# Kernel optimization log

Measured on AMD Instinct MI355X. Metric: run time of the kernel, lower is better.

## Reference

```python
import jax, jax.numpy as jnp
import numpy as np

WINDOW_SIZE = 11
SIGMA = 1.5
C1 = 0.01 ** 2
C2 = 0.03 ** 2
MSE_WEIGHT = 1.0
SSIM_WEIGHT = 0.01


def _gaussian_window(channels):
    # 1D gaussian, normalized, then outer product -> [C,1,K,K] depthwise kernel
    coords = np.arange(WINDOW_SIZE) - WINDOW_SIZE // 2
    g = np.exp(-(coords ** 2) / (2.0 * SIGMA ** 2))
    g = g / g.sum()
    w2d = np.outer(g, g).astype(np.float32)  # [K,K]
    w = np.tile(w2d[None, None], (channels, 1, 1, 1))  # [C,1,K,K]
    return jnp.asarray(w)


def _depthwise_conv(x, w):
    # x: [B,C,H,W], w: [C,1,K,K]; SAME padding, groups=C (matches torch conv2d pad=K//2, groups=C)
    pad = WINDOW_SIZE // 2
    return jax.lax.conv_general_dilated(
        x, w,
        window_strides=(1, 1),
        padding=[(pad, pad), (pad, pad)],
        dimension_numbers=('NCHW', 'OIHW', 'NCHW'),
        feature_group_count=x.shape[1],
    )


def setup_inputs() -> dict:
    key = jax.random.key(0)
    k1, k2 = jax.random.split(key)
    shape = (32, 3, 512, 512)
    predicted = jax.random.uniform(k1, shape, dtype=jnp.float32)
    target = jax.random.uniform(k2, shape, dtype=jnp.float32)
    return {"predicted": predicted, "target": target}


def reference(predicted, target):
    # MSE part
    mse_l = jnp.mean((predicted - target) ** 2)

    # SSIM part (standard pytorch-ssim: gaussian window, size_average=True)
    C = predicted.shape[1]
    w = _gaussian_window(C)

    mu1 = _depthwise_conv(predicted, w)
    mu2 = _depthwise_conv(target, w)
    mu1_sq = mu1 * mu1
    mu2_sq = mu2 * mu2
    mu1_mu2 = mu1 * mu2

    sigma1_sq = _depthwise_conv(predicted * predicted, w) - mu1_sq
    sigma2_sq = _depthwise_conv(target * target, w) - mu2_sq
    sigma12 = _depthwise_conv(predicted * target, w) - mu1_mu2

    ssim_map = ((2.0 * mu1_mu2 + C1) * (2.0 * sigma12 + C2)) / (
        (mu1_sq + mu2_sq + C1) * (sigma1_sq + sigma2_sq + C2)
    )
    ssim_val = jnp.mean(ssim_map)

    return MSE_WEIGHT * mse_l + SSIM_WEIGHT * (1.0 - ssim_val)
```

## Files before the change

### kernel.cpp

```cpp
#include <hip/hip_runtime.h>
#include <hip/hip_fp16.h>


#define WSZ   512
#define TW    64
#define TH    16
#define HALO  5
#define IN_H  (TH + 2*HALO)
#define NPOS  32
#define GX    (WSZ / TW)
#define GY    (WSZ / TH)
#define NSLOT 64
#define SSIM_C1 0.0001f
#define SSIM_C2 0.0009f

#define W0 0.00102838f
#define W1 0.00759876f
#define W2 0.03600080f
#define W3 0.10936080f
#define W4 0.21300560f
#define W5 0.26601170f
__device__ __constant__ const float GW[11] = {W0,W1,W2,W3,W4,W5,W4,W3,W2,W1,W0};

static __device__ __forceinline__ float pkh2(float a, float b) {
    return __builtin_bit_cast(float, __builtin_amdgcn_cvt_pkrtz(a, b));
}

__launch_bounds__(256, 8)
__global__ void fused_mse_ssim(const float* __restrict__ P,
                               const float* __restrict__ T,
                               float* __restrict__ ws) {
    __shared__ float4 sAB[IN_H][NPOS];
    __shared__ float  sC [IN_H][NPOS];
    __shared__ float  red[2][4];

    const int tid = threadIdx.x;
    const int gx0 = blockIdx.x * TW;
    const int gy0 = blockIdx.y * TH;
    const size_t plane = (size_t)blockIdx.z * (WSZ * (size_t)WSZ);
    const float* Pp = P + plane;
    const float* Tp = T + plane;

    float gw[11];
    #pragma unroll
    for (int k = 0; k < 11; ++k) gw[k] = GW[k];

    float mse = 0.f;

    for (int it = tid; it < IN_H * 16; it += 256) {
        const int r = it >> 4;
        const int q = it & 15;
        const int gy = gy0 - HALO + r;
        const int c0 = gx0 + q * 4 - 8;
        const bool rv = ((unsigned)gy < (unsigned)WSZ);
        const float* prow = Pp + (size_t)gy * WSZ;
        const float* trow = Tp + (size_t)gy * WSZ;

        float p[20], t[20];
        #pragma unroll
        for (int b = 0; b < 5; ++b) {
            const int c = c0 + 4 * b;
            float4 pv = make_float4(0.f, 0.f, 0.f, 0.f);
            float4 tv = make_float4(0.f, 0.f, 0.f, 0.f);
            if (rv && ((unsigned)c < (unsigned)WSZ)) {
                pv = *(const float4*)(prow + c);
                tv = *(const float4*)(trow + c);
            }
            p[4*b+0] = pv.x; p[4*b+1] = pv.y; p[4*b+2] = pv.z; p[4*b+3] = pv.w;
            t[4*b+0] = tv.x; t[4*b+1] = tv.y; t[4*b+2] = tv.z; t[4*b+3] = tv.w;
        }

        if ((unsigned)(r - HALO) < (unsigned)TH) {
            #pragma unroll
            for (int i = 0; i < 4; ++i) {
                const float d = p[8 + i] - t[8 + i];
                mse = fmaf(d, d, mse);
            }
        }

        float aP[4]  = {0.f,0.f,0.f,0.f};
        float aT[4]  = {0.f,0.f,0.f,0.f};
        float aPP[4] = {0.f,0.f,0.f,0.f};
        float aTT[4] = {0.f,0.f,0.f,0.f};
        float aPT[4] = {0.f,0.f,0.f,0.f};
        #pragma unroll
        for (int jj = 0; jj < 14; ++jj) {
            const float pv = p[jj + 3];
            const float tv = t[jj + 3];
            const float pp = pv * pv, tt2 = tv * tv, pt = pv * tv;
            #pragma unroll
            for (int o = 0; o < 4; ++o) {
                const int k = jj - o;
                if (k >= 0 && k < 11) {
                    const float w = gw[k];
                    aP[o]  = fmaf(w, pv,  aP[o]);
                    aT[o]  = fmaf(w, tv,  aT[o]);
                    aPP[o] = fmaf(w, pp,  aPP[o]);
                    aTT[o] = fmaf(w, tt2, aTT[o]);
                    aPT[o] = fmaf(w, pt,  aPT[o]);
                }
            }
        }

        sAB[r][2*q]   = make_float4(pkh2(aP[0], aP[1]), pkh2(aT[0], aT[1]),
                                    pkh2(aPP[0],aPP[1]), pkh2(aTT[0],aTT[1]));
        sAB[r][2*q+1] = make_float4(pkh2(aP[2], aP[3]), pkh2(aT[2], aT[3]),
                                    pkh2(aPP[2],aPP[3]), pkh2(aTT[2],aTT[3]));
        sC [r][2*q]   = pkh2(aPT[0], aPT[1]);
        sC [r][2*q+1] = pkh2(aPT[2], aPT[3]);
    }
    __syncthreads();

    __half2 gwh[11];
    #pragma unroll
    for (int k = 0; k < 11; ++k) gwh[k] = __float2half2_rn(gw[k]);

    const int q2 = tid & 31;
    const int y0 = (tid >> 5) * 2;

    __half2 acc[2][5];
    #pragma unroll
    for (int a = 0; a < 2; ++a)
        #pragma unroll
        for (int f = 0; f < 5; ++f)
            acc[a][f] = __float2half2_rn(0.f);

    #pragma unroll
    for (int j = 0; j < 12; ++j) {
        const float4 ab = sAB[y0 + j][q2];
        const float  cc = sC [y0 + j][q2];
        __half2 h[5];
        h[0] = __builtin_bit_cast(__half2, ab.x);
        h[1] = __builtin_bit_cast(__half2, ab.y);
        h[2] = __builtin_bit_cast(__half2, ab.z);
        h[3] = __builtin_bit_cast(__half2, ab.w);
        h[4] = __builtin_bit_cast(__half2, cc);
        if (j < 11) {
            #pragma unroll
            for (int f = 0; f < 5; ++f) acc[0][f] = __hfma2(gwh[j], h[f], acc[0][f]);
        }
        if (j >= 1) {
            #pragma unroll
            for (int f = 0; f < 5; ++f) acc[1][f] = __hfma2(gwh[j-1], h[f], acc[1][f]);
        }
    }

    float ssim = 0.f;
    #pragma unroll
    for (int a = 0; a < 2; ++a) {
        const float2 m1  = __half22float2(acc[a][0]);
        const float2 m2  = __half22float2(acc[a][1]);
        const float2 spp = __half22float2(acc[a][2]);
        const float2 stt = __half22float2(acc[a][3]);
        const float2 spt = __half22float2(acc[a][4]);
        #pragma unroll
        for (int e = 0; e < 2; ++e) {
            const float mu1 = e ? m1.y  : m1.x;
            const float mu2 = e ? m2.y  : m2.x;
            const float vpp = e ? spp.y : spp.x;
            const float vtt = e ? stt.y : stt.x;
            const float vpt = e ? spt.y : spt.x;
            const float mu1sq = mu1 * mu1;
            const float mu2sq = mu2 * mu2;
            const float mu12  = mu1 * mu2;
            const float s1  = vpp - mu1sq;
            const float s2  = vtt - mu2sq;
            const float s12 = vpt - mu12;
            const float num = fmaf(2.f, mu12, SSIM_C1) * fmaf(2.f, s12, SSIM_C2);
            const float den = (mu1sq + mu2sq + SSIM_C1) * (s1 + s2 + SSIM_C2);
            ssim = fmaf(num, __builtin_amdgcn_rcpf(den), ssim);
        }
    }

    #pragma unroll
    for (int off = 32; off > 0; off >>= 1) {
        mse  += __shfl_down(mse, off);
        ssim += __shfl_down(ssim, off);
    }
    const int wid = tid >> 6;
    if ((tid & 63) == 0) { red[0][wid] = mse; red[1][wid] = ssim; }
    __syncthreads();
    if (tid == 0) {
        const float m = red[0][0] + red[0][1] + red[0][2] + red[0][3];
        const float s = red[1][0] + red[1][1] + red[1][2] + red[1][3];
        const int bid  = (blockIdx.z * gridDim.y + blockIdx.y) * gridDim.x + blockIdx.x;
        const int slot = (bid & (NSLOT - 1)) * 16;
        atomicAdd(&ws[slot + 0], m);
        atomicAdd(&ws[slot + 1], s);
    }
}

__global__ void finalize_loss(const float* __restrict__ ws,
                              float* __restrict__ out, float invN) {
    const int t = threadIdx.x;
    float m = ws[t * 16 + 0];
    float s = ws[t * 16 + 1];
    #pragma unroll
    for (int off = 32; off > 0; off >>= 1) {
        m += __shfl_down(m, off);
        s += __shfl_down(s, off);
    }
    if (t == 0) out[0] = m * invN + 0.01f * (1.f - s * invN);
}

extern "C" void kernel_launch(void* const* d_in, const int* in_sizes, int n_in,
                              void* d_out, int out_size, void* d_ws, size_t ws_size,
                              hipStream_t stream) {
    const float* P = (const float*)d_in[0];
    const float* T = (const float*)d_in[1];
    float* out = (float*)d_out;
    float* ws  = (float*)d_ws;

    const int planes = in_sizes[0] / (WSZ * WSZ);
    const float invN = 1.f / (float)in_sizes[0];

    (void)hipMemsetAsync(ws, 0, NSLOT * 16 * sizeof(float), stream);
    dim3 grid(GX, GY, planes);
    fused_mse_ssim<<<grid, 256, 0, stream>>>(P, T, ws);
    finalize_loss<<<1, 64, 0, stream>>>(ws, out, invN);
}
```

Baseline: 266.4 us.

## Convolve sum/difference signals in packed half2 and double tile height

After: 234.3 us. 12.1% less time.

```diff
diff --git a/kernel.cpp b/kernel.cpp
--- a/kernel.cpp
+++ b/kernel.cpp
@@ -4,7 +4,7 @@
 
 #define WSZ   512
 #define TW    64
-#define TH    16
+#define TH    32
 #define HALO  5
 #define IN_H  (TH + 2*HALO)
 #define NPOS  32
@@ -20,18 +20,21 @@
 #define W3 0.10936080f
 #define W4 0.21300560f
 #define W5 0.26601170f
-__device__ __constant__ const float GW[11] = {W0,W1,W2,W3,W4,W5,W4,W3,W2,W1,W0};
-
-static __device__ __forceinline__ float pkh2(float a, float b) {
-    return __builtin_bit_cast(float, __builtin_amdgcn_cvt_pkrtz(a, b));
-}
-
-__launch_bounds__(256, 8)
+
+static __device__ __forceinline__ __half2 pk(float a, float b) {
+    return __builtin_bit_cast(__half2, __builtin_amdgcn_cvt_pkrtz(a, b));
+}
+static __device__ __forceinline__ __half2 stagger(__half2 hi, __half2 lo) {
+    return __builtin_bit_cast(__half2,
+        __builtin_amdgcn_alignbit(__builtin_bit_cast(unsigned, hi),
+                                  __builtin_bit_cast(unsigned, lo), 16));
+}
+
+__launch_bounds__(256, 6)
 __global__ void fused_mse_ssim(const float* __restrict__ P,
                                const float* __restrict__ T,
                                float* __restrict__ ws) {
     __shared__ float4 sAB[IN_H][NPOS];
-    __shared__ float  sC [IN_H][NPOS];
     __shared__ float  red[2][4];
 
     const int tid = threadIdx.x;
@@ -41,134 +44,162 @@
     const float* Pp = P + plane;
     const float* Tp = T + plane;
 
-    float gw[11];
-    #pragma unroll
-    for (int k = 0; k < 11; ++k) gw[k] = GW[k];
+    const float gwf[11] = {W0,W1,W2,W3,W4,W5,W4,W3,W2,W1,W0};
+    unsigned gwh[11];
+    #pragma unroll
+    for (int k = 0; k < 11; ++k)
+        gwh[k] = __builtin_amdgcn_readfirstlane(
+                     __builtin_bit_cast(unsigned, __float2half2_rn(gwf[k])));
 
     float mse = 0.f;
 
-    for (int it = tid; it < IN_H * 16; it += 256) {
-        const int r = it >> 4;
-        const int q = it & 15;
+    const bool interior = (blockIdx.x != 0) && (blockIdx.x != GX - 1) &&
+                          (blockIdx.y != 0) && (blockIdx.y != GY - 1);
+
+    for (int it = tid; it < IN_H * 8; it += 256) {
+        const int r  = it >> 3;
+        const int q  = it & 7;
         const int gy = gy0 - HALO + r;
-        const int c0 = gx0 + q * 4 - 8;
-        const bool rv = ((unsigned)gy < (unsigned)WSZ);
-        const float* prow = Pp + (size_t)gy * WSZ;
-        const float* trow = Tp + (size_t)gy * WSZ;
-
-        float p[20], t[20];
-        #pragma unroll
-        for (int b = 0; b < 5; ++b) {
-            const int c = c0 + 4 * b;
-            float4 pv = make_float4(0.f, 0.f, 0.f, 0.f);
-            float4 tv = make_float4(0.f, 0.f, 0.f, 0.f);
-            if (rv && ((unsigned)c < (unsigned)WSZ)) {
-                pv = *(const float4*)(prow + c);
-                tv = *(const float4*)(trow + c);
-            }
-            p[4*b+0] = pv.x; p[4*b+1] = pv.y; p[4*b+2] = pv.z; p[4*b+3] = pv.w;
-            t[4*b+0] = tv.x; t[4*b+1] = tv.y; t[4*b+2] = tv.z; t[4*b+3] = tv.w;
-        }
-
-        if ((unsigned)(r - HALO) < (unsigned)TH) {
+        const int cb = gx0 + q * 8 - 8;
+        const float* prow = Pp + ((long)gy * WSZ + cb);
+        const float* trow = Tp + ((long)gy * WSZ + cb);
+        const bool mrow = ((unsigned)(r - HALO) < (unsigned)TH);
+
+        __half2 As[12], Ad[12];
+
+        if (interior) {
             #pragma unroll
-            for (int i = 0; i < 4; ++i) {
-                const float d = p[8 + i] - t[8 + i];
-                mse = fmaf(d, d, mse);
-            }
-        }
-
-        float aP[4]  = {0.f,0.f,0.f,0.f};
-        float aT[4]  = {0.f,0.f,0.f,0.f};
-        float aPP[4] = {0.f,0.f,0.f,0.f};
-        float aTT[4] = {0.f,0.f,0.f,0.f};
-        float aPT[4] = {0.f,0.f,0.f,0.f};
-        #pragma unroll
-        for (int jj = 0; jj < 14; ++jj) {
-            const float pv = p[jj + 3];
-            const float tv = t[jj + 3];
-            const float pp = pv * pv, tt2 = tv * tv, pt = pv * tv;
+            for (int b = 0; b < 6; ++b) {
+                const float4 pv = *(const float4*)(prow + 4 * b);
+                const float4 tv = *(const float4*)(trow + 4 * b);
+                const float s0 = pv.x + tv.x, s1 = pv.y + tv.y;
+                const float s2 = pv.z + tv.z, s3 = pv.w + tv.w;
+                const float d0 = pv.x - tv.x, d1 = pv.y - tv.y;
+                const float d2 = pv.z - tv.z, d3 = pv.w - tv.w;
+                As[2*b]   = pk(s0, s1); As[2*b+1] = pk(s2, s3);
+                Ad[2*b]   = pk(d0, d1); Ad[2*b+1] = pk(d2, d3);
+                if ((b == 2 || b == 3) && mrow) {
+                    mse = fmaf(d0, d0, mse); mse = fmaf(d1, d1, mse);
+                    mse = fmaf(d2, d2, mse); mse = fmaf(d3, d3, mse);
+                }
+            }
+        } else {
+            const bool rv = ((unsigned)gy < (unsigned)WSZ);
             #pragma unroll
-            for (int o = 0; o < 4; ++o) {
-                const int k = jj - o;
+            for (int b = 0; b < 6; ++b) {
+                const unsigned c = (unsigned)(cb + 4 * b);
+                float4 pv = make_float4(0.f, 0.f, 0.f, 0.f);
+                float4 tv = make_float4(0.f, 0.f, 0.f, 0.f);
+                if (rv && c < (unsigned)WSZ) {
+                    pv = *(const float4*)(prow + 4 * b);
+                    tv = *(const float4*)(trow + 4 * b);
+                }
+                const float s0 = pv.x + tv.x, s1 = pv.y + tv.y;
+                const float s2 = pv.z + tv.z, s3 = pv.w + tv.w;
+                const float d0 = pv.x - tv.x, d1 = pv.y - tv.y;
+                const float d2 = pv.z - tv.z, d3 = pv.w - tv.w;
+                As[2*b]   = pk(s0, s1); As[2*b+1] = pk(s2, s3);
+                Ad[2*b]   = pk(d0, d1); Ad[2*b+1] = pk(d2, d3);
+                if ((b == 2 || b == 3) && mrow) {
+                    mse = fmaf(d0, d0, mse); mse = fmaf(d1, d1, mse);
+                    mse = fmaf(d2, d2, mse); mse = fmaf(d3, d3, mse);
+                }
+            }
+        }
+
+        const __half2 z = __float2half2_rn(0.f);
+        __half2 aS[4]  = {z, z, z, z};
+        __half2 aD[4]  = {z, z, z, z};
+        __half2 aSS[4] = {z, z, z, z};
+        __half2 aDD[4] = {z, z, z, z};
+
+        #pragma unroll
+        for (int jj = 0; jj <= 16; ++jj) {
+            const int j = jj + 3;
+            __half2 vs, vd;
+            if (j & 1) {
+                vs = stagger(As[(j >> 1) + 1], As[j >> 1]);
+                vd = stagger(Ad[(j >> 1) + 1], Ad[j >> 1]);
+            } else {
+                vs = As[j >> 1];
+                vd = Ad[j >> 1];
+            }
+            const __half2 vss = __hmul2(vs, vs);
+            const __half2 vdd = __hmul2(vd, vd);
+            #pragma unroll
+            for (int m = 0; m < 4; ++m) {
+                const int k = jj - 2 * m;
                 if (k >= 0 && k < 11) {
-                    const float w = gw[k];
-                    aP[o]  = fmaf(w, pv,  aP[o]);
-                    aT[o]  = fmaf(w, tv,  aT[o]);
-                    aPP[o] = fmaf(w, pp,  aPP[o]);
-                    aTT[o] = fmaf(w, tt2, aTT[o]);
-                    aPT[o] = fmaf(w, pt,  aPT[o]);
-                }
-            }
-        }
-
-        sAB[r][2*q]   = make_float4(pkh2(aP[0], aP[1]), pkh2(aT[0], aT[1]),
-                                    pkh2(aPP[0],aPP[1]), pkh2(aTT[0],aTT[1]));
-        sAB[r][2*q+1] = make_float4(pkh2(aP[2], aP[3]), pkh2(aT[2], aT[3]),
-                                    pkh2(aPP[2],aPP[3]), pkh2(aTT[2],aTT[3]));
-        sC [r][2*q]   = pkh2(aPT[0], aPT[1]);
-        sC [r][2*q+1] = pkh2(aPT[2], aPT[3]);
+                    const __half2 w = __builtin_bit_cast(__half2, gwh[k]);
+                    aS[m]  = __hfma2(w, vs,  aS[m]);
+                    aD[m]  = __hfma2(w, vd,  aD[m]);
+                    aSS[m] = __hfma2(w, vss, aSS[m]);
+                    aDD[m] = __hfma2(w, vdd, aDD[m]);
+                }
+            }
+        }
+
+        #pragma unroll
+        for (int m = 0; m < 4; ++m)
+            sAB[r][8 * m + q] = make_float4(
+                __builtin_bit_cast(float, aS[m]),  __builtin_bit_cast(float, aD[m]),
+                __builtin_bit_cast(float, aSS[m]), __builtin_bit_cast(float, aDD[m]));
     }
     __syncthreads();
 
-    __half2 gwh[11];
-    #pragma unroll
-    for (int k = 0; k < 11; ++k) gwh[k] = __float2half2_rn(gw[k]);
-
-    const int q2 = tid & 31;
-    const int y0 = (tid >> 5) * 2;
-
-    __half2 acc[2][5];
-    #pragma unroll
-    for (int a = 0; a < 2; ++a)
-        #pragma unroll
-        for (int f = 0; f < 5; ++f)
-            acc[a][f] = __float2half2_rn(0.f);
-
-    #pragma unroll
-    for (int j = 0; j < 12; ++j) {
-        const float4 ab = sAB[y0 + j][q2];
-        const float  cc = sC [y0 + j][q2];
-        __half2 h[5];
-        h[0] = __builtin_bit_cast(__half2, ab.x);
-        h[1] = __builtin_bit_cast(__half2, ab.y);
-        h[2] = __builtin_bit_cast(__half2, ab.z);
-        h[3] = __builtin_bit_cast(__half2, ab.w);
-        h[4] = __builtin_bit_cast(__half2, cc);
-        if (j < 11) {
-            #pragma unroll
-            for (int f = 0; f < 5; ++f) acc[0][f] = __hfma2(gwh[j], h[f], acc[0][f]);
-        }
-        if (j >= 1) {
-            #pragma unroll
-            for (int f = 0; f < 5; ++f) acc[1][f] = __hfma2(gwh[j-1], h[f], acc[1][f]);
+    const int q2  = tid & 31;
+    const int col = ((q2 & 3) << 3) | (q2 >> 2);
+    const int y0  = (tid >> 5) << 2;
+
+    const __half2 z2 = __float2half2_rn(0.f);
+    __half2 acc[4][4];
+    #pragma unroll
+    for (int a = 0; a < 4; ++a) {
+        acc[a][0] = z2; acc[a][1] = z2; acc[a][2] = z2; acc[a][3] = z2;
+    }
+
+    #pragma unroll
+    for (int j = 0; j < 14; ++j) {
+        const float4 ab = sAB[y0 + j][col];
+        const __half2 hS  = __builtin_bit_cast(__half2, ab.x);
+        const __half2 hD  = __builtin_bit_cast(__half2, ab.y);
+        const __half2 hSS = __builtin_bit_cast(__half2, ab.z);
+        const __half2 hDD = __builtin_bit_cast(__half2, ab.w);
+        #pragma unroll
+        for (int a = 0; a < 4; ++a) {
+            const int k = j - a;
+            if (k >= 0 && k < 11) {
+                const __half2 w = __builtin_bit_cast(__half2, gwh[k]);
+                acc[a][0] = __hfma2(w, hS,  acc[a][0]);
+                acc[a][1] = __hfma2(w, hD,  acc[a][1]);
+                acc[a][2] = __hfma2(w, hSS, acc[a][2]);
+                acc[a][3] = __hfma2(w, hDD, acc[a][3]);
+            }
         }
     }
 
     float ssim = 0.f;
     #pragma unroll
-    for (int a = 0; a < 2; ++a) {
-        const float2 m1  = __half22float2(acc[a][0]);
-        const float2 m2  = __half22float2(acc[a][1]);
-        const float2 spp = __half22float2(acc[a][2]);
-        const float2 stt = __half22float2(acc[a][3]);
-        const float2 spt = __half22float2(acc[a][4]);
+    for (int a = 0; a < 4; ++a) {
+        const float2 Av = __half22float2(acc[a][0]);
+        const float2 Bv = __half22float2(acc[a][1]);
+        const float2 Xv = __half22float2(acc[a][2]);
+        const float2 Yv = __half22float2(acc[a][3]);
         #pragma unroll
         for (int e = 0; e < 2; ++e) {
-            const float mu1 = e ? m1.y  : m1.x;
-            const float mu2 = e ? m2.y  : m2.x;
-            const float vpp = e ? spp.y : spp.x;
-            const float vtt = e ? stt.y : stt.x;
-            const float vpt = e ? spt.y : spt.x;
-            const float mu1sq = mu1 * mu1;
-            const float mu2sq = mu2 * mu2;
-            const float mu12  = mu1 * mu2;
-            const float s1  = vpp - mu1sq;
-            const float s2  = vtt - mu2sq;
-            const float s12 = vpt - mu12;
-            const float num = fmaf(2.f, mu12, SSIM_C1) * fmaf(2.f, s12, SSIM_C2);
-            const float den = (mu1sq + mu2sq + SSIM_C1) * (s1 + s2 + SSIM_C2);
-            ssim = fmaf(num, __builtin_amdgcn_rcpf(den), ssim);
+            const float A = e ? Av.y : Av.x;
+            const float B = e ? Bv.y : Bv.x;
+            const float X = e ? Xv.y : Xv.x;
+            const float Y = e ? Yv.y : Yv.x;
+            const float a2 = A * A;
+            const float b2 = B * B;
+            const float P1 = a2 + b2;
+            const float M1 = a2 - b2;
+            const float num1 = fmaf(0.5f, M1, SSIM_C1);
+            const float den1 = fmaf(0.5f, P1, SSIM_C1);
+            const float num2 = fmaf(0.5f, (X - Y) - M1, SSIM_C2);
+            const float den2 = fmaf(0.5f, (X + Y) - P1, SSIM_C2);
+            ssim = fmaf(num1 * num2, __builtin_amdgcn_rcpf(den1 * den2), ssim);
         }
     }
 
```
